# Kernel optimization log

Hardware: AMD Instinct MI355X
Metric: run time of the kernel (lower is better)

Reference implementation:

```python
import jax, jax.numpy as jnp
import numpy as np

NUM_COMPONENTS = 4
HEADS = 24
DIM_HEAD = 64
EPS = 1e-8

def setup_inputs() -> dict:
    key = jax.random.key(0)
    ks = jax.random.split(key, 6)
    BC, S, D = 8, 4096, 1536   # batch*components, spatial tokens, hidden dim
    T = 154                     # encoder (text) sequence length
    w_scale = D ** -0.5
    return {
        "hidden_states": jax.random.normal(ks[0], (BC, S, D), jnp.float32),
        "encoder_hidden_states": jax.random.normal(ks[1], (BC, T, D), jnp.float32),
        "Wq": jax.random.normal(ks[2], (D, D), jnp.float32) * w_scale,
        "bq": jnp.zeros((D,), jnp.float32),
        "Wk": jax.random.normal(ks[3], (D, D), jnp.float32) * w_scale,
        "bk": jnp.zeros((D,), jnp.float32),
        "Wv": jax.random.normal(ks[4], (D, D), jnp.float32) * w_scale,
        "bv": jnp.zeros((D,), jnp.float32),
        "Wo": jax.random.normal(ks[5], (D, D), jnp.float32) * w_scale,
        "bo": jnp.zeros((D,), jnp.float32),
    }

def reference(hidden_states, encoder_hidden_states, Wq, bq, Wk, bk, Wv, bv, Wo, bo):
    BC, S, D = hidden_states.shape
    T = encoder_hidden_states.shape[1]
    C = NUM_COMPONENTS
    B = BC // C
    H, dh = HEADS, DIM_HEAD
    scale = dh ** -0.5

    # linear projections (torch Linear: x @ W.T + b)
    q = hidden_states @ Wq.T + bq            # [BC, S, D]
    k = encoder_hidden_states @ Wk.T + bk     # [BC, T, D]
    v = encoder_hidden_states @ Wv.T + bv     # [BC, T, D]

    q = q.reshape(BC, S, H, dh).transpose(0, 2, 1, 3)  # [BC, H, S, dh]
    k = k.reshape(BC, T, H, dh).transpose(0, 2, 1, 3)  # [BC, H, T, dh]
    v = v.reshape(BC, T, H, dh).transpose(0, 2, 1, 3)  # [BC, H, T, dh]

    # full score tensor, softmax over the COMPONENT axis, then renormalize over keys
    scores = jnp.einsum('bhsd,bhtd->bhst', q, k) * scale        # [BC, H, S, T]
    scores = scores.reshape(C, B, H, S, T)
    w = jax.nn.softmax(scores, axis=0).reshape(BC, H, S, T)
    w = w / (jnp.sum(w, axis=-1, keepdims=True) + EPS)

    out = jnp.einsum('bhst,bhtd->bhsd', w, v)                   # [BC, H, S, dh]
    out = out.transpose(0, 2, 1, 3).reshape(BC, S, D)
    out = out @ Wo.T + bo
    return out
```

## Files before the change

kernel.cpp:

```cpp
#include <hip/hip_runtime.h>


typedef unsigned short u16;
typedef unsigned int   u32;

#define NHS   50331648ULL
#define NEHS  1892352ULL
#define NW    2359296ULL
#define NVT   1966080ULL

using bf16x8 = __attribute__((ext_vector_type(8))) short;
using f32x4  = __attribute__((ext_vector_type(4))) float;

__device__ __forceinline__ u16 f2bf(float f) {
  union { float f; u32 u; } x{f};
  u32 r = (x.u + 0x7fffu + ((x.u >> 16) & 1u)) >> 16;
  return (u16)r;
}

__device__ __forceinline__ void gload_lds16(const u16* g, u16* s) {
  __builtin_amdgcn_global_load_lds((const __attribute__((address_space(1))) void*)g,
                                   (__attribute__((address_space(3))) void*)s,
                                   16, 0, 0);
}

#define WAITV(N) asm volatile("s_waitcnt vmcnt(" #N ")" ::: "memory")

__global__ void cvt_bf16(const float* __restrict__ src, u16* __restrict__ dst, int n4) {
  int idx = blockIdx.x * blockDim.x + threadIdx.x;
  int stride = gridDim.x * blockDim.x;
  for (int i = idx; i < n4; i += stride) {
    float4 v = ((const float4*)src)[i];
    ushort4 o;
    o.x = f2bf(v.x); o.y = f2bf(v.y); o.z = f2bf(v.z); o.w = f2bf(v.w);
    ((ushort4*)dst)[i] = o;
  }
}

template <int MODE>
__global__ __launch_bounds__(512, 2)
void gemm_big(const u16* __restrict__ Ag, const u16* __restrict__ Bw,
              const float* __restrict__ bias, void* __restrict__ Cv) {
  __shared__ __align__(16) u16 lds[65536];

  const int tid  = threadIdx.x;
  const int wv   = tid >> 6;
  const int lane = tid & 63;
  const int l16  = lane & 15, quad = lane >> 4;
  const int wm = wv >> 2, wn = wv & 3;

  const int wg = ((int)blockIdx.x & 7) * 96 + ((int)blockIdx.x >> 3);
  const int by = wg & 127;
  const int bx = wg >> 7;
  const int m0 = by * 256, n0 = bx * 256;

  const u16* gsrc[4];
  int ldst[4];
#pragma unroll
  for (int q = 0; q < 4; ++q) {
    const int L = q * 512 + tid;
    const int cid = L & 1023;
    const int row = cid >> 2;
    const int csrc = ((L & 3) ^ ((row >> 1) & 3)) * 8;
    gsrc[q] = (L < 1024 ? Ag + (size_t)(m0 + row) * 1536
                        : Bw + (size_t)(n0 + row) * 1536) + csrc;
    ldst[q] = L * 8;
  }

  int aoff[8], boff[4];
#pragma unroll
  for (int i = 0; i < 8; ++i) {
    const int ra = wm * 128 + i * 16 + l16;
    aoff[i] = ra * 32 + ((quad ^ ((ra >> 1) & 3)) * 8);
  }
#pragma unroll
  for (int j = 0; j < 4; ++j) {
    const int rb = wn * 64 + j * 16 + l16;
    boff[j] = 8192 + rb * 32 + ((quad ^ ((rb >> 1) & 3)) * 8);
  }

  f32x4 acc[8][4];
#pragma unroll
  for (int i = 0; i < 8; ++i)
#pragma unroll
    for (int j = 0; j < 4; ++j) acc[i][j] = {0.f, 0.f, 0.f, 0.f};

  auto stage = [&](int tile) {
    u16* dst = &lds[(tile & 3) * 16384];
    const int kt = tile * 32;
#pragma unroll
    for (int q = 0; q < 4; ++q)
      gload_lds16(gsrc[q] + kt, dst + ldst[q]);
  };

  auto compute = [&](int tile) {
    const u16* buf = &lds[(tile & 3) * 16384];
    __builtin_amdgcn_s_setprio(1);
    bf16x8 bfr[4];
#pragma unroll
    for (int j = 0; j < 4; ++j) bfr[j] = *(const bf16x8*)&buf[boff[j]];
#pragma unroll
    for (int i = 0; i < 8; ++i) {
      bf16x8 af = *(const bf16x8*)&buf[aoff[i]];
#pragma unroll
      for (int j = 0; j < 4; ++j)
        acc[i][j] = __builtin_amdgcn_mfma_f32_16x16x32_bf16(af, bfr[j], acc[i][j], 0, 0, 0);
    }
    __builtin_amdgcn_s_setprio(0);
  };

  stage(0); stage(1); stage(2);
  WAITV(8);
  __builtin_amdgcn_s_barrier();

  for (int t = 0; t < 45; ++t) {
    stage(t + 3);
    compute(t);
    WAITV(8);
    __builtin_amdgcn_s_barrier();
  }
  compute(45); WAITV(4); __builtin_amdgcn_s_barrier();
  compute(46); WAITV(0); __builtin_amdgcn_s_barrier();
  compute(47);

#pragma unroll
  for (int i = 0; i < 8; ++i) {
    const int row0 = m0 + wm * 128 + i * 16 + quad * 4;
#pragma unroll
    for (int j = 0; j < 4; ++j) {
      const int col = n0 + wn * 64 + j * 16 + l16;
      const float bvs = bias[col];
#pragma unroll
      for (int rr = 0; rr < 4; ++rr) {
        const int row = row0 + rr;
        const float v = acc[i][j][rr] + bvs;
        if (MODE == 0) ((float*)Cv)[(size_t)row * 1536 + col] = v;
        else           ((u16*)Cv)[(size_t)row * 1536 + col] = f2bf(v);
      }
    }
  }
}

template <int MODE>
__global__ __launch_bounds__(256)
void gemm_bt(const u16* __restrict__ A, const u16* __restrict__ Bw,
             const float* __restrict__ bias, void* __restrict__ Cv,
             int M, int K) {
  const int N = 1536;
  __shared__ __align__(16) u16 As[4096];
  __shared__ __align__(16) u16 Bs[4096];
  const int tid  = threadIdx.x;
  const int wv   = tid >> 6;
  const int lane = tid & 63;
  const int wr = wv >> 1, wc = wv & 1;
  const int l16 = lane & 15, quad = lane >> 4;
  const int m0 = blockIdx.y * 128, n0 = blockIdx.x * 128;
  const int r = tid >> 2, c8 = (tid & 3) * 8;

  int ra0 = m0 + r;      if (ra0 > M - 1) ra0 = M - 1;
  int ra1 = m0 + 64 + r; if (ra1 > M - 1) ra1 = M - 1;
  const u16* a0 = A  + (size_t)ra0 * K + c8;
  const u16* a1 = A  + (size_t)ra1 * K + c8;
  const u16* b0 = Bw + (size_t)(n0 + r) * K + c8;
  const u16* b1 = Bw + (size_t)(n0 + 64 + r) * K + c8;
  u16* asd0 = &As[tid * 8];
  u16* asd1 = &As[2048 + tid * 8];
  u16* bsd0 = &Bs[tid * 8];
  u16* bsd1 = &Bs[2048 + tid * 8];

  f32x4 acc[4][4];
#pragma unroll
  for (int i = 0; i < 4; ++i)
#pragma unroll
    for (int j = 0; j < 4; ++j) acc[i][j] = {0.f, 0.f, 0.f, 0.f};

  for (int kt = 0; kt < K; kt += 32) {
    __syncthreads();
    gload_lds16(a0 + kt, asd0);
    gload_lds16(a1 + kt, asd1);
    gload_lds16(b0 + kt, bsd0);
    gload_lds16(b1 + kt, bsd1);
    __syncthreads();
    bf16x8 af[4], bfr[4];
#pragma unroll
    for (int i = 0; i < 4; ++i) {
      af[i]  = *(const bf16x8*)&As[(wr * 64 + i * 16 + l16) * 32 + quad * 8];
      bfr[i] = *(const bf16x8*)&Bs[(wc * 64 + i * 16 + l16) * 32 + quad * 8];
    }
#pragma unroll
    for (int i = 0; i < 4; ++i)
#pragma unroll
      for (int j = 0; j < 4; ++j)
        acc[i][j] = __builtin_amdgcn_mfma_f32_16x16x32_bf16(af[i], bfr[j], acc[i][j], 0, 0, 0);
  }

#pragma unroll
  for (int i = 0; i < 4; ++i) {
    const int rb = m0 + wr * 64 + i * 16 + quad * 4;
#pragma unroll
    for (int j = 0; j < 4; ++j) {
      const int col = n0 + wc * 64 + j * 16 + l16;
      const float bvs = bias[col];
#pragma unroll
      for (int rr = 0; rr < 4; ++rr) {
        const int row = rb + rr;
        if (row < M) {
          float v = acc[i][j][rr] + bvs;
          if (MODE == 1) {
            ((u16*)Cv)[(size_t)row * N + col] = f2bf(v);
          } else {
            const int bc = row / 154;
            const int t  = row - bc * 154;
            ((u16*)Cv)[((size_t)bc * 1536 + col) * 160 + t] = f2bf(v);
          }
        }
      }
    }
  }
}

__global__ __launch_bounds__(256, 2)
void attn_kernel(const u16* __restrict__ qg, const u16* __restrict__ kg,
                 const u16* __restrict__ vtg, u16* __restrict__ og) {
  __shared__ __align__(16) u16 lds[40960];

  const int tid  = threadIdx.x;
  const int wv   = tid >> 6;
  const int lane = tid & 63;
  const int l16 = lane & 15, quad = lane >> 4;
  const int s0 = blockIdx.x * 64;
  const int h  = blockIdx.y;
  const int b  = blockIdx.z;
  const int swz = ((quad ^ ((l16 >> 1) & 3)) * 8);

  {
    const u16* kbase = kg + (size_t)b * 154 * 1536 + h * 64;
#pragma unroll
    for (int p = 0; p < 20; ++p) {
      const int L = p * 256 + tid;
      const int r = L >> 2;
      const int t = r % 160;
      const int cks = r / 160;
      const int c = cks >> 1, ks = cks & 1;
      const int csrc = ((L & 3) ^ ((t >> 1) & 3)) * 8;
      const u16* src = kbase + ((size_t)c * 308 + t) * 1536 + ks * 32 + csrc;
      gload_lds16(src, &lds[(size_t)L * 8]);
    }
  }

  bf16x8 qa[4][2];
#pragma unroll
  for (int c = 0; c < 4; ++c) {
    const u16* qrow = qg + ((size_t)((c * 2 + b) * 4096 + s0 + wv * 16 + l16)) * 1536 + h * 64;
#pragma unroll
    for (int ks = 0; ks < 2; ++ks)
      qa[c][ks] = *(const bf16x8*)(qrow + ks * 32 + quad * 8);
  }
  __syncthreads();

  f32x4 sc[4][10];
#pragma unroll
  for (int c = 0; c < 4; ++c)
#pragma unroll
    for (int nt = 0; nt < 10; ++nt) sc[c][nt] = {0.f, 0.f, 0.f, 0.f};

#pragma unroll
  for (int nt = 0; nt < 10; ++nt)
#pragma unroll
    for (int c = 0; c < 4; ++c)
#pragma unroll
      for (int ks = 0; ks < 2; ++ks) {
        bf16x8 kf = *(const bf16x8*)&lds[((c * 2 + ks) * 160 + nt * 16 + l16) * 32 + swz];
        sc[c][nt] = __builtin_amdgcn_mfma_f32_16x16x32_bf16(qa[c][ks], kf, sc[c][nt], 0, 0, 0);
      }

  float rs[4][4];
#pragma unroll
  for (int c = 0; c < 4; ++c)
#pragma unroll
    for (int rr = 0; rr < 4; ++rr) rs[c][rr] = 0.f;

#pragma unroll
  for (int nt = 0; nt < 10; ++nt) {
    const int t = nt * 16 + l16;
    const bool ok = (t < 154);
#pragma unroll
    for (int rr = 0; rr < 4; ++rr) {
      float v0 = sc[0][nt][rr] * 0.125f;
      float v1 = sc[1][nt][rr] * 0.125f;
      float v2 = sc[2][nt][rr] * 0.125f;
      float v3 = sc[3][nt][rr] * 0.125f;
      float m = fmaxf(fmaxf(v0, v1), fmaxf(v2, v3));
      float e0 = __expf(v0 - m), e1 = __expf(v1 - m);
      float e2 = __expf(v2 - m), e3 = __expf(v3 - m);
      float inv = 1.f / (e0 + e1 + e2 + e3);
      float w0 = ok ? e0 * inv : 0.f;
      float w1 = ok ? e1 * inv : 0.f;
      float w2 = ok ? e2 * inv : 0.f;
      float w3 = ok ? e3 * inv : 0.f;
      sc[0][nt][rr] = w0; sc[1][nt][rr] = w1; sc[2][nt][rr] = w2; sc[3][nt][rr] = w3;
      rs[0][rr] += w0; rs[1][rr] += w1; rs[2][rr] += w2; rs[3][rr] += w3;
    }
  }
#pragma unroll
  for (int c = 0; c < 4; ++c)
#pragma unroll
    for (int rr = 0; rr < 4; ++rr) {
      float v = rs[c][rr];
      v += __shfl_xor(v, 1); v += __shfl_xor(v, 2);
      v += __shfl_xor(v, 4); v += __shfl_xor(v, 8);
      rs[c][rr] = 1.f / (v + 1e-8f);
    }

  __syncthreads();

  const u16* vbase = vtg + ((size_t)b * 1536 + h * 64) * 160;

  auto stage_v = [&](int c, int par) {
    const u16* vb = vbase + (size_t)c * 2 * 1536 * 160;
    u16* slot = &lds[20480 + par * 10240];
#pragma unroll
    for (int p = 0; p < 5; ++p) {
      const int L = p * 256 + tid;
      const int row = L >> 2;
      const int ks = row >> 6, dh = row & 63;
      const int csrc = ((L & 3) ^ ((dh >> 1) & 3)) * 8;
      gload_lds16(vb + dh * 160 + ks * 32 + csrc, &slot[(size_t)L * 8]);
    }
  };

  auto write_w = [&](int c, int par) {
    u16* slot = &lds[par * 10240];
#pragma unroll
    for (int nt = 0; nt < 10; ++nt) {
#pragma unroll
      for (int rr = 0; rr < 4; ++rr) {
        const int srow = wv * 16 + quad * 4 + rr;
        const int t = nt * 16 + l16;
        const int cl = ((t >> 3) & 3) ^ ((srow >> 1) & 3);
        slot[srow * 160 + (t >> 5) * 32 + cl * 8 + (t & 7)] =
            f2bf(sc[c][nt][rr] * rs[c][rr]);
      }
    }
  };

  f32x4 oacc[4][4];
#pragma unroll
  for (int c = 0; c < 4; ++c)
#pragma unroll
    for (int nd = 0; nd < 4; ++nd) oacc[c][nd] = {0.f, 0.f, 0.f, 0.f};

  stage_v(0, 0);
  write_w(0, 0);
#pragma unroll
  for (int c = 0; c < 4; ++c) {
    __syncthreads();
    if (c < 3) { stage_v(c + 1, (c + 1) & 1); write_w(c + 1, (c + 1) & 1); }
    const int par = c & 1;
    const u16* sw = &lds[par * 10240];
    const u16* sv = &lds[20480 + par * 10240];
#pragma unroll
    for (int ks = 0; ks < 5; ++ks) {
      bf16x8 wa = *(const bf16x8*)&sw[(wv * 16 + l16) * 160 + ks * 32 + swz];
#pragma unroll
      for (int nd = 0; nd < 4; ++nd) {
        bf16x8 vf = *(const bf16x8*)&sv[(ks * 64 + nd * 16 + l16) * 32 + swz];
        oacc[c][nd] = __builtin_amdgcn_mfma_f32_16x16x32_bf16(wa, vf, oacc[c][nd], 0, 0, 0);
      }
    }
  }

#pragma unroll
  for (int c = 0; c < 4; ++c)
#pragma unroll
    for (int nd = 0; nd < 4; ++nd)
#pragma unroll
      for (int rr = 0; rr < 4; ++rr) {
        const int srow = s0 + wv * 16 + quad * 4 + rr;
        og[((size_t)((c * 2 + b) * 4096 + srow)) * 1536 + h * 64 + nd * 16 + l16] =
            f2bf(oacc[c][nd][rr]);
      }
}

extern "C" void kernel_launch(void* const* d_in, const int* in_sizes, int n_in,
                              void* d_out, int out_size, void* d_ws, size_t ws_size,
                              hipStream_t stream) {
  (void)in_sizes; (void)n_in; (void)out_size; (void)ws_size;
  const float* hs  = (const float*)d_in[0];
  const float* ehs = (const float*)d_in[1];
  const float* Wq  = (const float*)d_in[2];
  const float* bq  = (const float*)d_in[3];
  const float* Wk  = (const float*)d_in[4];
  const float* bk  = (const float*)d_in[5];
  const float* Wv  = (const float*)d_in[6];
  const float* bv  = (const float*)d_in[7];
  const float* Wo  = (const float*)d_in[8];
  const float* bo  = (const float*)d_in[9];
  float* out = (float*)d_out;

  u16* ws   = (u16*)d_ws;
  u16* hsb  = ws;
  u16* ehsb = hsb + NHS;
  u16* wqb  = ehsb + NEHS;
  u16* wkb  = wqb + NW;
  u16* wvb  = wkb + NW;
  u16* wob  = wvb + NW;
  u16* qb   = wob + NW;
  u16* kgb  = qb + NHS;
  u16* vtb  = kgb + NEHS;
  u16* atb  = vtb + NVT;

  auto cvt = [&](const float* s, u16* d, size_t n) {
    int n4 = (int)(n / 4);
    int blocks = (n4 + 255) / 256;
    if (blocks > 8192) blocks = 8192;
    cvt_bf16<<<blocks, 256, 0, stream>>>(s, d, n4);
  };
  cvt(hs, hsb, NHS);
  cvt(ehs, ehsb, NEHS);
  cvt(Wq, wqb, NW);
  cvt(Wk, wkb, NW);
  cvt(Wv, wvb, NW);
  cvt(Wo, wob, NW);

  gemm_big<1><<<dim3(768), 512, 0, stream>>>(hsb, wqb, bq, qb);
  gemm_bt<1><<<dim3(12, 10), 256, 0, stream>>>(ehsb, wkb, bk, kgb, 1232, 1536);
  gemm_bt<2><<<dim3(12, 10), 256, 0, stream>>>(ehsb, wvb, bv, vtb, 1232, 1536);

  attn_kernel<<<dim3(64, 24, 2), 256, 0, stream>>>(qb, kgb, vtb, atb);

  gemm_big<0><<<dim3(768), 512, 0, stream>>>(atb, wob, bo, out);
}
```

Baseline: 909.4 us.

## Split GEMM k-tile into two half-phases interleaving LDS reads, prefetch and MFMA

Restructures the GEMM main loop so each k-tile is processed in two halves: load B fragments and half of the A fragments, issue half of the global-to-LDS prefetch, barrier, run 16 MFMAs, then repeat for the other half. This is meant to interleave memory issue with matrix work across waves and cut register pressure from holding all A fragments at once. In exchange it adds extra barriers per tile, which may add synchronisation stalls.

```diff
diff --git a/kernel.cpp b/kernel.cpp
--- a/kernel.cpp
+++ b/kernel.cpp
@@ -85,43 +85,56 @@
 #pragma unroll
     for (int j = 0; j < 4; ++j) acc[i][j] = {0.f, 0.f, 0.f, 0.f};
 
-  auto stage = [&](int tile) {
+  auto stage2 = [&](int tile, int qb) {
     u16* dst = &lds[(tile & 3) * 16384];
     const int kt = tile * 32;
-#pragma unroll
-    for (int q = 0; q < 4; ++q)
-      gload_lds16(gsrc[q] + kt, dst + ldst[q]);
+    gload_lds16(gsrc[qb] + kt, dst + ldst[qb]);
+    gload_lds16(gsrc[qb + 1] + kt, dst + ldst[qb + 1]);
   };
 
-  auto compute = [&](int tile) {
-    const u16* buf = &lds[(tile & 3) * 16384];
-    __builtin_amdgcn_s_setprio(1);
-    bf16x8 bfr[4];
-#pragma unroll
-    for (int j = 0; j < 4; ++j) bfr[j] = *(const bf16x8*)&buf[boff[j]];
-#pragma unroll
-    for (int i = 0; i < 8; ++i) {
-      bf16x8 af = *(const bf16x8*)&buf[aoff[i]];
-#pragma unroll
-      for (int j = 0; j < 4; ++j)
-        acc[i][j] = __builtin_amdgcn_mfma_f32_16x16x32_bf16(af, bfr[j], acc[i][j], 0, 0, 0);
-    }
-    __builtin_amdgcn_s_setprio(0);
-  };
-
-  stage(0); stage(1); stage(2);
+#define TILE_BODY(T, DO_STAGE, WAITCODE)                                      \
+  {                                                                           \
+    const u16* buf = &lds[((T) & 3) * 16384];                                 \
+    bf16x8 bfr[4], af[4];                                                     \
+    _Pragma("unroll") for (int j = 0; j < 4; ++j)                             \
+      bfr[j] = *(const bf16x8*)&buf[boff[j]];                                 \
+    _Pragma("unroll") for (int i = 0; i < 4; ++i)                             \
+      af[i] = *(const bf16x8*)&buf[aoff[i]];                                  \
+    if (DO_STAGE) stage2((T) + 3, 0);                                         \
+    __builtin_amdgcn_s_barrier();                                             \
+    __builtin_amdgcn_s_setprio(1);                                            \
+    _Pragma("unroll") for (int i = 0; i < 4; ++i)                             \
+      _Pragma("unroll") for (int j = 0; j < 4; ++j)                           \
+        acc[i][j] = __builtin_amdgcn_mfma_f32_16x16x32_bf16(af[i], bfr[j],    \
+                                                            acc[i][j], 0, 0, 0); \
+    __builtin_amdgcn_s_setprio(0);                                            \
+    __builtin_amdgcn_s_barrier();                                             \
+    _Pragma("unroll") for (int i = 0; i < 4; ++i)                             \
+      af[i] = *(const bf16x8*)&buf[aoff[4 + i]];                              \
+    if (DO_STAGE) stage2((T) + 3, 2);                                         \
+    __builtin_amdgcn_s_barrier();                                             \
+    __builtin_amdgcn_s_setprio(1);                                            \
+    _Pragma("unroll") for (int i = 0; i < 4; ++i)                             \
+      _Pragma("unroll") for (int j = 0; j < 4; ++j)                           \
+        acc[4 + i][j] = __builtin_amdgcn_mfma_f32_16x16x32_bf16(af[i], bfr[j],\
+                                                        acc[4 + i][j], 0, 0, 0); \
+    __builtin_amdgcn_s_setprio(0);                                            \
+    WAITCODE;                                                                 \
+    __builtin_amdgcn_s_barrier();                                             \
+  }
+
+  stage2(0, 0); stage2(0, 2);
+  stage2(1, 0); stage2(1, 2);
+  stage2(2, 0); stage2(2, 2);
   WAITV(8);
   __builtin_amdgcn_s_barrier();
 
-  for (int t = 0; t < 45; ++t) {
-    stage(t + 3);
-    compute(t);
-    WAITV(8);
-    __builtin_amdgcn_s_barrier();
-  }
-  compute(45); WAITV(4); __builtin_amdgcn_s_barrier();
-  compute(46); WAITV(0); __builtin_amdgcn_s_barrier();
-  compute(47);
+  for (int t = 0; t < 45; ++t)
+    TILE_BODY(t, true, WAITV(8));
+  TILE_BODY(45, false, WAITV(4));
+  TILE_BODY(46, false, WAITV(0));
+  TILE_BODY(47, false, (void)0);
+#undef TILE_BODY
 
 #pragma unroll
   for (int i = 0; i < 8; ++i) {
```

Result: no change. 904.1 us (-0.6%).

## Restructure big GEMM main loop with 64-wide K tiles and interleaved double buffering

Applied to the files above, without the earlier changes.

The projection GEMM kernel moves from 32-wide K tiles in a 4-slot ring buffer to 64-wide K tiles in two LDS buffers, with a new XOR swizzle for the wider rows. Each tile is split into four sub-phases that interleave LDS fragment reads, async global-to-LDS staging of the next tile and 16-MFMA bursts, separated by barriers and explicit lgkmcnt waits. The goal is better overlap of global loads, LDS reads and MFMA work, with fewer loop iterations. In exchange it adds many more barriers per tile and a full vmcnt(0) drain every tile, which could expose memory latency.

```diff
diff --git a/kernel.cpp b/kernel.cpp
--- a/kernel.cpp
+++ b/kernel.cpp
@@ -25,6 +25,8 @@
 }
 
 #define WAITV(N) asm volatile("s_waitcnt vmcnt(" #N ")" ::: "memory")
+#define LGKM(N)  do { asm volatile("s_waitcnt lgkmcnt(" #N ")" ::: "memory"); \
+                      __builtin_amdgcn_sched_barrier(0); } while (0)
 
 __global__ void cvt_bf16(const float* __restrict__ src, u16* __restrict__ dst, int n4) {
   int idx = blockIdx.x * blockDim.x + threadIdx.x;
@@ -54,29 +56,23 @@
   const int bx = wg >> 7;
   const int m0 = by * 256, n0 = bx * 256;
 
-  const u16* gsrc[4];
-  int ldst[4];
-#pragma unroll
-  for (int q = 0; q < 4; ++q) {
-    const int L = q * 512 + tid;
-    const int cid = L & 1023;
-    const int row = cid >> 2;
-    const int csrc = ((L & 3) ^ ((row >> 1) & 3)) * 8;
-    gsrc[q] = (L < 1024 ? Ag + (size_t)(m0 + row) * 1536
-                        : Bw + (size_t)(n0 + row) * 1536) + csrc;
-    ldst[q] = L * 8;
-  }
-
-  int aoff[8], boff[4];
-#pragma unroll
-  for (int i = 0; i < 8; ++i) {
-    const int ra = wm * 128 + i * 16 + l16;
-    aoff[i] = ra * 32 + ((quad ^ ((ra >> 1) & 3)) * 8);
-  }
-#pragma unroll
-  for (int j = 0; j < 4; ++j) {
-    const int rb = wn * 64 + j * 16 + l16;
-    boff[j] = 8192 + rb * 32 + ((quad ^ ((rb >> 1) & 3)) * 8);
+  int soff[4];
+#pragma unroll
+  for (int i = 0; i < 4; ++i) {
+    const int c = i * 512 + tid;
+    const int row = c >> 3;
+    soff[i] = row * 1536 + (((c & 7) ^ (row & 7)) * 8);
+  }
+  const u16* Abp = Ag + (size_t)m0 * 1536;
+  const u16* Bbp = Bw + (size_t)n0 * 1536;
+  const int ldst = tid * 8;
+
+  int aoffb[2], boffb[2];
+#pragma unroll
+  for (int ks = 0; ks < 2; ++ks) {
+    const int ch = ((ks * 4 + quad) ^ (l16 & 7)) * 8;
+    aoffb[ks] = (wm * 128 + l16) * 64 + ch;
+    boffb[ks] = 16384 + (wn * 64 + l16) * 64 + ch;
   }
 
   f32x4 acc[8][4];
@@ -85,43 +81,72 @@
 #pragma unroll
     for (int j = 0; j < 4; ++j) acc[i][j] = {0.f, 0.f, 0.f, 0.f};
 
-  auto stage = [&](int tile) {
-    u16* dst = &lds[(tile & 3) * 16384];
-    const int kt = tile * 32;
-#pragma unroll
-    for (int q = 0; q < 4; ++q)
-      gload_lds16(gsrc[q] + kt, dst + ldst[q]);
-  };
-
-  auto compute = [&](int tile) {
-    const u16* buf = &lds[(tile & 3) * 16384];
-    __builtin_amdgcn_s_setprio(1);
-    bf16x8 bfr[4];
-#pragma unroll
-    for (int j = 0; j < 4; ++j) bfr[j] = *(const bf16x8*)&buf[boff[j]];
-#pragma unroll
-    for (int i = 0; i < 8; ++i) {
-      bf16x8 af = *(const bf16x8*)&buf[aoff[i]];
-#pragma unroll
-      for (int j = 0; j < 4; ++j)
-        acc[i][j] = __builtin_amdgcn_mfma_f32_16x16x32_bf16(af, bfr[j], acc[i][j], 0, 0, 0);
-    }
-    __builtin_amdgcn_s_setprio(0);
-  };
-
-  stage(0); stage(1); stage(2);
-  WAITV(8);
-  __builtin_amdgcn_s_barrier();
-
-  for (int t = 0; t < 45; ++t) {
-    stage(t + 3);
-    compute(t);
-    WAITV(8);
-    __builtin_amdgcn_s_barrier();
-  }
-  compute(45); WAITV(4); __builtin_amdgcn_s_barrier();
-  compute(46); WAITV(0); __builtin_amdgcn_s_barrier();
-  compute(47);
+  bf16x8 af[4], bf[4];
+
+#define STG_A(TN, BN) do {                                                    \
+    gload_lds16(Abp + soff[0] + (TN) * 64, &lds[(BN) + ldst]);                \
+    gload_lds16(Abp + soff[1] + (TN) * 64, &lds[(BN) + 4096 + ldst]);         \
+    gload_lds16(Abp + soff[2] + (TN) * 64, &lds[(BN) + 8192 + ldst]);         \
+    gload_lds16(Abp + soff[3] + (TN) * 64, &lds[(BN) + 12288 + ldst]);        \
+  } while (0)
+#define STG_B(TN, BN) do {                                                    \
+    gload_lds16(Bbp + soff[0] + (TN) * 64, &lds[(BN) + 16384 + ldst]);        \
+    gload_lds16(Bbp + soff[1] + (TN) * 64, &lds[(BN) + 20480 + ldst]);        \
+    gload_lds16(Bbp + soff[2] + (TN) * 64, &lds[(BN) + 24576 + ldst]);        \
+    gload_lds16(Bbp + soff[3] + (TN) * 64, &lds[(BN) + 28672 + ldst]);        \
+  } while (0)
+#define RD_AF(BC, KS, RH)                                                     \
+    _Pragma("unroll") for (int i = 0; i < 4; ++i)                             \
+      af[i] = *(const bf16x8*)&lds[(BC) + aoffb[KS] + (RH) * 4096 + i * 1024]
+#define RD_BF(BC, KS)                                                         \
+    _Pragma("unroll") for (int j = 0; j < 4; ++j)                             \
+      bf[j] = *(const bf16x8*)&lds[(BC) + boffb[KS] + j * 1024]
+#define MM16(RH)                                                              \
+    __builtin_amdgcn_s_setprio(1);                                            \
+    _Pragma("unroll") for (int i = 0; i < 4; ++i)                             \
+      _Pragma("unroll") for (int j = 0; j < 4; ++j)                           \
+        acc[(RH) * 4 + i][j] = __builtin_amdgcn_mfma_f32_16x16x32_bf16(       \
+            af[i], bf[j], acc[(RH) * 4 + i][j], 0, 0, 0);                     \
+    __builtin_amdgcn_s_setprio(0)
+#define BAR __builtin_amdgcn_s_barrier()
+
+#define TILE(BC, BN, TN, DOST, DOWAIT) do {                                   \
+                                                           \
+    RD_BF(BC, 0); RD_AF(BC, 0, 0);                                            \
+    if (DOST) STG_A(TN, BN);                                                  \
+    BAR; LGKM(0); MM16(0); BAR;                                               \
+                                                           \
+    RD_AF(BC, 0, 1);                                                          \
+    if (DOST) STG_B(TN, BN);                                                  \
+    BAR; LGKM(0); MM16(1); BAR;                                               \
+                                                           \
+    RD_BF(BC, 1); RD_AF(BC, 1, 0);                                            \
+    BAR; LGKM(0); MM16(0); BAR;                                               \
+                                                           \
+    RD_AF(BC, 1, 1);                                                          \
+    BAR; LGKM(0); MM16(1);                                                    \
+    if (DOWAIT) WAITV(0);                                                     \
+    BAR;                                                                      \
+  } while (0)
+
+  STG_A(0, 0); STG_B(0, 0);
+  WAITV(0);
+  BAR;
+
+  for (int t = 0; t < 22; t += 2) {
+    TILE(0,     32768, t + 1, true, true);
+    TILE(32768, 0,     t + 2, true, true);
+  }
+  TILE(0,     32768, 23, true, true);
+  TILE(32768, 0,     24, false, false);
+
+#undef TILE
+#undef BAR
+#undef MM16
+#undef RD_BF
+#undef RD_AF
+#undef STG_B
+#undef STG_A
 
 #pragma unroll
   for (int i = 0; i < 8; ++i) {
```

Measured after the change: 883.6 us. -2.8%, faster.
